# Kernel tuning notes

Hardware: AMD Instinct MI355X
Metric: run time of the kernel (lower is better)

Reference implementation:

```python
import jax, jax.numpy as jnp
import numpy as np

D_MODEL = 256
NHEAD = 8
D_K = D_MODEL // NHEAD
IM_SIZE = 8
SCALE = float(IM_SIZE ** 2)  # sqrt(im_size**4)


def setup_inputs() -> dict:
    key = jax.random.key(0)
    ks = jax.random.split(key, 9)
    B, P, S = 8, 256, 8
    s = 1.0 / np.sqrt(D_MODEL)
    return {
        "x": jax.random.normal(ks[0], (B, P, S, S, D_MODEL), jnp.float32),
        "Wq": jax.random.normal(ks[1], (D_MODEL, D_MODEL), jnp.float32) * s,
        "bq": jax.random.normal(ks[2], (D_MODEL,), jnp.float32) * s,
        "Wk": jax.random.normal(ks[3], (D_MODEL, D_MODEL), jnp.float32) * s,
        "bk": jax.random.normal(ks[4], (D_MODEL,), jnp.float32) * s,
        "Wv": jax.random.normal(ks[5], (D_MODEL, D_MODEL), jnp.float32) * s,
        "bv": jax.random.normal(ks[6], (D_MODEL,), jnp.float32) * s,
        "Wo": jax.random.normal(ks[7], (D_MODEL, D_MODEL), jnp.float32) * s,
        "bo": jax.random.normal(ks[8], (D_MODEL,), jnp.float32) * s,
    }


def _split_heads(t):
    # torch: view(..., d_k, nhead).permute(0,5,1,2,3,4) -> [b, n, p, x, y, d_k]
    b, p, sx, sy, _ = t.shape
    t = t.reshape(b, p, sx, sy, D_K, NHEAD)
    return jnp.transpose(t, (0, 5, 1, 2, 3, 4))


def reference(x, Wq, bq, Wk, bk, Wv, bv, Wo, bo):
    Q = _split_heads(x @ Wq.T + bq)
    K = _split_heads(x @ Wk.T + bk)
    V = _split_heads(x @ Wv.T + bv)
    # scores over flattened (x, y, d_k) dims
    scores = jnp.einsum('bnpxyd,bnqxyd->bnpq', Q, K) / SCALE
    attn = jax.nn.softmax(scores, axis=-1)
    out = jnp.einsum('bnpq,bnqxyd->bnpxyd', attn, V)
    # permute to [b, p, x, y, d_k, n] then merge (d_k, n) -> d_model
    out = jnp.transpose(out, (0, 2, 3, 4, 5, 1))
    b, p, sx, sy, _, _ = out.shape
    out = out.reshape(b, p, sx, sy, NHEAD * D_K)
    return out @ Wo.T + bo
```

## Files before the change

kernel.cpp:

```cpp
#include <hip/hip_runtime.h>
#include <hip/hip_bf16.h>


typedef __bf16 bf16;
typedef __attribute__((ext_vector_type(8))) __bf16 bf16x8;
typedef __attribute__((ext_vector_type(4))) float floatx4;
typedef __attribute__((ext_vector_type(8))) unsigned short ushort8;

#define CDIM 2048

static __device__ __forceinline__ floatx4 mfma16(bf16x8 a, bf16x8 b, floatx4 c) {
  return __builtin_amdgcn_mfma_f32_16x16x32_bf16(a, b, c, 0, 0, 0);
}

static __device__ __forceinline__ void gload_lds16(const void* g, void* l) {
  __builtin_amdgcn_global_load_lds((const __attribute__((address_space(1))) void*)g,
                                   (__attribute__((address_space(3))) void*)l, 16, 0, 0);
}

__global__ __launch_bounds__(256) void k0_prep(
    const float* __restrict__ Wq, const float* __restrict__ bq,
    const float* __restrict__ Wk, const float* __restrict__ bk,
    const float* __restrict__ Wv, const float* __restrict__ bv,
    const float* __restrict__ Wo,
    bf16* __restrict__ Wp, bf16* __restrict__ Wk3, float* __restrict__ biasp)
{
  const int bid = blockIdx.x, tid = threadIdx.x;
  int g = (bid & 31) * 256 + tid;
  int lane = g & 63, rowblk = (g >> 6) & 15, kk = g >> 10;
  int h = lane >> 4, cl = lane & 15;
  int d0 = kk * 32 + 8 * h;
  if (bid < 32) {
    int ip = rowblk * 16 + cl;
    int isrc = ((ip & 31) << 3) | (ip >> 5);
#pragma unroll
    for (int mat = 0; mat < 3; mat++) {
      const float* W = (mat == 0) ? Wq : (mat == 1) ? Wk : Wv;
      bf16x8 v;
#pragma unroll
      for (int j = 0; j < 8; j++) v[j] = (bf16)W[isrc * 256 + d0 + j];
      *reinterpret_cast<bf16x8*>(Wp + ((size_t)mat * 8192 + g) * 8) = v;
    }
    if (bid == 0 && tid < 256) {
      int bs = ((tid & 31) << 3) | (tid >> 5);
      biasp[tid] = bq[bs]; biasp[256 + tid] = bk[bs]; biasp[512 + tid] = bv[bs];
    }
  } else {
    int j = rowblk * 16 + cl;
    bf16x8 v;
#pragma unroll
    for (int jj = 0; jj < 8; jj++) {
      int c = d0 + jj;
      v[jj] = (bf16)Wo[j * 256 + (((c & 31) << 3) | (c >> 5))];
    }
    *reinterpret_cast<bf16x8*>(Wk3 + (size_t)g * 8) = v;
  }
}

__global__ __launch_bounds__(512, 4) void k1_qkv(
    const float* __restrict__ x, const bf16* __restrict__ Wp,
    const float* __restrict__ biasp,
    bf16* __restrict__ Qs, bf16* __restrict__ Ks, bf16* __restrict__ Vt)
{
  __shared__ bf16 buf[2][64 * 256];
  const int bx = blockIdx.x;
  const int tid = threadIdx.x;
  const int lane = tid & 63;
  const int w = tid >> 6;
  const int h = lane >> 4, cl = lane & 15;
  const int c7 = cl & 7;

  floatx4 sreg[8];

#define K1_LOAD(VB)                                                          \
  {                                                                          \
    int a_ = (VB) / 24;                                                      \
    int t0_ = (a_ * 8 + ((VB) & 7)) * 64;                                    \
    _Pragma("unroll")                                                        \
    for (int k = 0; k < 4; ++k) {                                            \
      int G = k * 512 + tid;                                                 \
      int row = G >> 5;                                                      \
      const float* sp = x + (size_t)(t0_ + row) * 256 + (G & 31) * 8;        \
      sreg[2 * k]     = *reinterpret_cast<const floatx4*>(sp);               \
      sreg[2 * k + 1] = *reinterpret_cast<const floatx4*>(sp + 4);           \
    }                                                                        \
  }

#define K1_CVTWRITE(BUFI)                                                    \
  {                                                                          \
    _Pragma("unroll")                                                        \
    for (int k = 0; k < 4; ++k) {                                            \
      int G = k * 512 + tid;                                                 \
      int row = G >> 5;                                                      \
      bf16x8 v;                                                              \
      _Pragma("unroll")                                                      \
      for (int j = 0; j < 4; j++) {                                          \
        v[j] = (bf16)sreg[2 * k][j];                                         \
        v[4 + j] = (bf16)sreg[2 * k + 1][j];                                 \
      }                                                                      \
      int Gp = (G & ~7) | ((G ^ row) & 7);                                   \
      *reinterpret_cast<bf16x8*>(&buf[BUFI][Gp * 8]) = v;                    \
    }                                                                        \
  }

#define K1_COMPUTE(VB, BUFI)                                                 \
  {                                                                          \
    int a_ = (VB) / 24;                                                      \
    int rem_ = (VB) - a_ * 24;                                               \
    int mat_ = rem_ >> 3;                                                    \
    int t0_ = (a_ * 8 + (rem_ & 7)) * 64;                                    \
    const bf16* Wm = Wp + (size_t)mat_ * 65536;                              \
    floatx4 acc[4][2];                                                       \
    _Pragma("unroll")                                                        \
    for (int i = 0; i < 4; i++)                                              \
      _Pragma("unroll")                                                      \
      for (int j = 0; j < 2; j++) acc[i][j] = (floatx4)0.0f;                 \
    _Pragma("unroll 2")                                                      \
    for (int kk = 0; kk < 8; ++kk) {                                         \
      bf16x8 av[4];                                                          \
      _Pragma("unroll")                                                      \
      for (int mt = 0; mt < 4; mt++) {                                       \
        int rr = mt * 16 + cl;                                               \
        int G = rr * 32 + kk * 4 + h;                                        \
        int Gp = (G & ~7) | ((G ^ c7) & 7);                                  \
        av[mt] = *reinterpret_cast<const bf16x8*>(&buf[BUFI][Gp * 8]);       \
      }                                                                      \
      bf16x8 b0 = *reinterpret_cast<const bf16x8*>(                          \
          Wm + ((size_t)(kk * 16 + w * 2 + 0) * 64 + lane) * 8);             \
      bf16x8 b1 = *reinterpret_cast<const bf16x8*>(                          \
          Wm + ((size_t)(kk * 16 + w * 2 + 1) * 64 + lane) * 8);             \
      _Pragma("unroll")                                                      \
      for (int mt = 0; mt < 4; mt++) acc[mt][0] = mfma16(av[mt], b0, acc[mt][0]); \
      _Pragma("unroll")                                                      \
      for (int mt = 0; mt < 4; mt++) acc[mt][1] = mfma16(av[mt], b1, acc[mt][1]); \
    }                                                                        \
    int b_ = t0_ >> 14;                                                      \
    int p_ = (t0_ >> 6) & 255;                                               \
    if (mat_ < 2) {                                                          \
      bf16* ob = ((mat_ == 0) ? Qs : Ks) + ((size_t)(b_ * 8 + w) * 256 + p_) * 2048; \
      _Pragma("unroll")                                                      \
      for (int nt = 0; nt < 2; nt++) {                                       \
        const int ip = w * 32 + nt * 16 + cl;                                \
        const float bb = biasp[mat_ * 256 + ip];                             \
        const int dk = nt * 16 + cl;                                         \
        _Pragma("unroll")                                                    \
        for (int mt = 0; mt < 4; mt++)                                       \
          _Pragma("unroll")                                                  \
          for (int r = 0; r < 4; r++) {                                      \
            int sxy = mt * 16 + 4 * h + r;                                   \
            ob[sxy * 32 + dk] = (bf16)(acc[mt][nt][r] + bb);                 \
          }                                                                  \
      }                                                                      \
    } else {                                                                 \
      _Pragma("unroll")                                                      \
      for (int nt = 0; nt < 2; nt++) {                                       \
        const int ip = w * 32 + nt * 16 + cl;                                \
        const float bb = biasp[512 + ip];                                    \
        _Pragma("unroll")                                                    \
        for (int mt = 0; mt < 4; mt++)                                       \
          _Pragma("unroll")                                                  \
          for (int r = 0; r < 4; r++) {                                      \
            int t = t0_ + mt * 16 + 4 * h + r;                               \
            Vt[(size_t)t * 256 + ip] = (bf16)(acc[mt][nt][r] + bb);          \
          }                                                                  \
      }                                                                      \
    }                                                                        \
  }

  K1_LOAD(bx);
  K1_CVTWRITE(0);
  __syncthreads();
#pragma unroll
  for (int u = 1; u < 4; ++u) {
    K1_LOAD(bx + u * 1536);
    K1_COMPUTE(bx + (u - 1) * 1536, (u - 1) & 1);
    __syncthreads();
    K1_CVTWRITE(u & 1);
    __syncthreads();
  }
  K1_COMPUTE(bx + 3 * 1536, 1);

#undef K1_LOAD
#undef K1_CVTWRITE
#undef K1_COMPUTE
}

__global__ __launch_bounds__(1024, 4) void k2a_scores(
    const bf16* __restrict__ Qs, const bf16* __restrict__ Ks,
    bf16* __restrict__ attn)
{
  __shared__ bf16 Qch[2][128 * 64];
  __shared__ bf16 Kch[2][256 * 64];
  __shared__ float redmax[4][4][32];
  __shared__ float redsum[4][4][32];

  const int bx = blockIdx.x;
  const int bn = bx & 63;
  const int p0 = (bx >> 6) * 128;
  const int tid = threadIdx.x;
  const int lane = tid & 63;
  const int w = tid >> 6;
  const int wr = w >> 2, wc = w & 3;
  const int h = lane >> 4, cl = lane & 15;

  const bf16* Qb = Qs + (size_t)bn * 524288 + (size_t)p0 * 2048;
  const bf16* Kb = Ks + (size_t)bn * 524288;

  const int Lq = w * 64 + lane;
  const int rq = Lq >> 3, sq = (Lq & 7) ^ (rq & 7);
  const size_t qsrc = (size_t)rq * 2048 + sq * 8;
  int rk[2]; size_t ksrc[2];
#pragma unroll
  for (int i = 0; i < 2; ++i) {
    int L = i * 1024 + w * 64 + lane;
    rk[i] = L >> 3;
    int s = (L & 7) ^ (rk[i] & 7);
    ksrc[i] = (size_t)rk[i] * 2048 + s * 8;
  }

#define K2A_STAGE(bufi, c)                                                  \
  {                                                                         \
    gload_lds16(Qb + qsrc + (c) * 64, &Qch[bufi][(w * 64) * 8]);            \
    gload_lds16(Kb + ksrc[0] + (c) * 64, &Kch[bufi][(w * 64) * 8]);         \
    gload_lds16(Kb + ksrc[1] + (c) * 64, &Kch[bufi][(1024 + w * 64) * 8]);  \
  }

  floatx4 acc[2][4];
#pragma unroll
  for (int i = 0; i < 2; i++)
#pragma unroll
    for (int j = 0; j < 4; j++) acc[i][j] = (floatx4)0.0f;

  K2A_STAGE(0, 0);
  __syncthreads();
  int buf = 0;
  for (int c = 0; c < 32; ++c) {
    if (c + 1 < 32) K2A_STAGE(buf ^ 1, c + 1);
#pragma unroll
    for (int kk = 0; kk < 2; ++kk) {
      bf16x8 av[2], bv[4];
#pragma unroll
      for (int mt = 0; mt < 2; mt++) {
        int row = wr * 32 + mt * 16 + cl;
        int gg = kk * 4 + h;
        av[mt] = *reinterpret_cast<const bf16x8*>(
            &Qch[buf][(row * 8 + (gg ^ (row & 7))) * 8]);
      }
#pragma unroll
      for (int nt = 0; nt < 4; nt++) {
        int row = wc * 64 + nt * 16 + cl;
        int gg = kk * 4 + h;
        bv[nt] = *reinterpret_cast<const bf16x8*>(
            &Kch[buf][(row * 8 + (gg ^ (row & 7))) * 8]);
      }
#pragma unroll
      for (int nt = 0; nt < 4; nt++)
#pragma unroll
        for (int mt = 0; mt < 2; mt++)
          acc[mt][nt] = mfma16(av[mt], bv[nt], acc[mt][nt]);
    }
    __syncthreads();
    buf ^= 1;
  }

  float pm[2][4];
#pragma unroll
  for (int mt = 0; mt < 2; mt++)
#pragma unroll
    for (int r = 0; r < 4; r++)
      pm[mt][r] = fmaxf(fmaxf(acc[mt][0][r], acc[mt][1][r]),
                        fmaxf(acc[mt][2][r], acc[mt][3][r]));
#pragma unroll
  for (int off = 1; off < 16; off <<= 1)
#pragma unroll
    for (int mt = 0; mt < 2; mt++)
#pragma unroll
      for (int r = 0; r < 4; r++)
        pm[mt][r] = fmaxf(pm[mt][r], __shfl_xor(pm[mt][r], off, 64));
  if (cl == 0) {
#pragma unroll
    for (int mt = 0; mt < 2; mt++)
#pragma unroll
      for (int r = 0; r < 4; r++) redmax[wr][wc][mt * 16 + 4 * h + r] = pm[mt][r];
  }
  __syncthreads();

  float gm[2][4], ps[2][4];
#pragma unroll
  for (int mt = 0; mt < 2; mt++)
#pragma unroll
    for (int r = 0; r < 4; r++) {
      int row = mt * 16 + 4 * h + r;
      gm[mt][r] = fmaxf(fmaxf(redmax[wr][0][row], redmax[wr][1][row]),
                        fmaxf(redmax[wr][2][row], redmax[wr][3][row]));
      ps[mt][r] = 0.0f;
    }
  const float KS = 1.44269504088896340736f / 64.0f;
#pragma unroll
  for (int mt = 0; mt < 2; mt++)
#pragma unroll
    for (int nt = 0; nt < 4; nt++)
#pragma unroll
      for (int r = 0; r < 4; r++) {
        float e = exp2f((acc[mt][nt][r] - gm[mt][r]) * KS);
        acc[mt][nt][r] = e;
        ps[mt][r] += e;
      }
#pragma unroll
  for (int off = 1; off < 16; off <<= 1)
#pragma unroll
    for (int mt = 0; mt < 2; mt++)
#pragma unroll
      for (int r = 0; r < 4; r++) ps[mt][r] += __shfl_xor(ps[mt][r], off, 64);
  if (cl == 0) {
#pragma unroll
    for (int mt = 0; mt < 2; mt++)
#pragma unroll
      for (int r = 0; r < 4; r++) redsum[wr][wc][mt * 16 + 4 * h + r] = ps[mt][r];
  }
  __syncthreads();

#pragma unroll
  for (int mt = 0; mt < 2; mt++)
#pragma unroll
    for (int r = 0; r < 4; r++) {
      int row = mt * 16 + 4 * h + r;
      float gs = (redsum[wr][0][row] + redsum[wr][1][row])
               + (redsum[wr][2][row] + redsum[wr][3][row]);
      ps[mt][r] = 1.0f / gs;
    }
#pragma unroll
  for (int nt = 0; nt < 4; nt++) {
    int q = wc * 64 + nt * 16 + cl;
#pragma unroll
    for (int mt = 0; mt < 2; mt++)
#pragma unroll
      for (int r = 0; r < 4; r++) {
        int row = p0 + wr * 32 + mt * 16 + 4 * h + r;
        attn[(size_t)bn * 65536 + row * 256 + q] = (bf16)(acc[mt][nt][r] * ps[mt][r]);
      }
  }
#undef K2A_STAGE
}

__global__ __launch_bounds__(256) void k2t_transpose(
    const bf16* __restrict__ Vtok, bf16* __restrict__ Vq)
{
  const int bx = blockIdx.x;
  const int bn = bx & 63;
  const int r2 = bx >> 6;
  const int q0 = (r2 & 3) * 64;
  const int c0 = (r2 >> 2) * 64;
  const int b = bn >> 3, n = bn & 7;
  __shared__ unsigned short tile[64][65];
  const unsigned short* src = (const unsigned short*)Vtok;
  unsigned short* dst = (unsigned short*)Vq + (size_t)bn * 524288;
  {
    const int q = threadIdx.x >> 3;
    const int cj = (threadIdx.x & 7) * 8;
    const int c = c0 + cj;
    const int sxy = c >> 5, dk0 = c & 31;
#pragma unroll
    for (int it = 0; it < 2; ++it) {
      int qq = q + it * 32;
      size_t sa = (size_t)((b * 256 + q0 + qq) * 64 + sxy) * 256 + n * 32 + dk0;
      ushort8 s = *reinterpret_cast<const ushort8*>(src + sa);
#pragma unroll
      for (int j = 0; j < 8; j++) tile[qq][cj + j] = s[j];
    }
  }
  __syncthreads();
  {
    const int crow = threadIdx.x >> 2;
    const int qj = (threadIdx.x & 3) * 8;
#pragma unroll
    for (int it = 0; it < 2; ++it) {
      int qq = qj + it * 32;
      ushort8 sv;
#pragma unroll
      for (int j = 0; j < 8; j++) sv[j] = tile[qq + j][crow];
      *reinterpret_cast<ushort8*>(dst + (size_t)(c0 + crow) * 256 + q0 + qq) = sv;
    }
  }
}

__global__ __launch_bounds__(512, 6) void k2b_pv(
    const bf16* __restrict__ attn, const bf16* __restrict__ Vq,
    bf16* __restrict__ yhat)
{
  __shared__ bf16 As[64 * 256];
  const int bx = blockIdx.x;
  const int bn = bx & 63;
  const int r2 = bx >> 6;
  const int p0 = (r2 & 3) * 64;
  const int c0 = (r2 >> 2) * 256;
  const int b = bn >> 3, n = bn & 7;
  const int tid = threadIdx.x;
  const int lane = tid & 63;
  const int w = tid >> 6;
  const int h = lane >> 4, cl = lane & 15;
  const int c7 = cl & 7;

  const bf16* Ab = attn + (size_t)bn * 65536 + (size_t)p0 * 256;
  const bf16* Vb = Vq + (size_t)bn * 524288;

#pragma unroll
  for (int i = 0; i < 4; ++i) {
    int L = (i * 8 + w) * 64 + lane;
    int S = (L & ~7) | ((L ^ (L >> 5)) & 7);
    gload_lds16(Ab + (size_t)S * 8, &As[(size_t)(i * 8 + w) * 64 * 8]);
  }
  __syncthreads();

  floatx4 acc[4][2];
#pragma unroll
  for (int i = 0; i < 4; i++)
#pragma unroll
    for (int j = 0; j < 2; j++) acc[i][j] = (floatx4)0.0f;

#pragma unroll 2
  for (int kk = 0; kk < 8; ++kk) {
    bf16x8 av[4];
#pragma unroll
    for (int mt = 0; mt < 4; mt++) {
      int rr = mt * 16 + cl;
      int G = rr * 32 + kk * 4 + h;
      int Gp = (G & ~7) | ((G ^ c7) & 7);
      av[mt] = *reinterpret_cast<const bf16x8*>(&As[Gp * 8]);
    }
    bf16x8 b0 = *reinterpret_cast<const bf16x8*>(
        Vb + (size_t)(c0 + w * 32 + cl) * 256 + kk * 32 + 8 * h);
    bf16x8 b1 = *reinterpret_cast<const bf16x8*>(
        Vb + (size_t)(c0 + w * 32 + 16 + cl) * 256 + kk * 32 + 8 * h);
#pragma unroll
    for (int mt = 0; mt < 4; mt++) acc[mt][0] = mfma16(av[mt], b0, acc[mt][0]);
#pragma unroll
    for (int mt = 0; mt < 4; mt++) acc[mt][1] = mfma16(av[mt], b1, acc[mt][1]);
  }

#pragma unroll
  for (int nt = 0; nt < 2; nt++) {
    const int cg = c0 + w * 32 + nt * 16 + cl;
    const int dk = cg & 31, sxy = cg >> 5;
#pragma unroll
    for (int mt = 0; mt < 4; mt++)
#pragma unroll
      for (int r = 0; r < 4; r++) {
        int p = p0 + mt * 16 + 4 * h + r;
        size_t t = (size_t)((b * 256 + p) * 64) + sxy;
        yhat[t * 256 + n * 32 + dk] = (bf16)acc[mt][nt][r];
      }
  }
}

__global__ __launch_bounds__(512, 6) void k3_out(
    const bf16* __restrict__ yhat, const bf16* __restrict__ Wk3,
    const float* __restrict__ bo, float* __restrict__ outp)
{
  __shared__ bf16 As[64 * 256];
  const int t0 = blockIdx.x * 64;
  const int tid = threadIdx.x;
  const int lane = tid & 63;
  const int w = tid >> 6;
  const int h = lane >> 4, cl = lane & 15;
  const int c7 = cl & 7;

  const bf16* Ab = yhat + (size_t)t0 * 256;

#pragma unroll
  for (int i = 0; i < 4; ++i) {
    int L = (i * 8 + w) * 64 + lane;
    int S = (L & ~7) | ((L ^ (L >> 5)) & 7);
    gload_lds16(Ab + (size_t)S * 8, &As[(size_t)(i * 8 + w) * 64 * 8]);
  }
  __syncthreads();

  floatx4 acc[4][2];
#pragma unroll
  for (int i = 0; i < 4; i++)
#pragma unroll
    for (int j = 0; j < 2; j++) acc[i][j] = (floatx4)0.0f;

#pragma unroll 2
  for (int kk = 0; kk < 8; ++kk) {
    bf16x8 av[4];
#pragma unroll
    for (int mt = 0; mt < 4; mt++) {
      int rr = mt * 16 + cl;
      int G = rr * 32 + kk * 4 + h;
      int Gp = (G & ~7) | ((G ^ c7) & 7);
      av[mt] = *reinterpret_cast<const bf16x8*>(&As[Gp * 8]);
    }
    bf16x8 b0 = *reinterpret_cast<const bf16x8*>(
        Wk3 + ((size_t)(kk * 16 + w * 2 + 0) * 64 + lane) * 8);
    bf16x8 b1 = *reinterpret_cast<const bf16x8*>(
        Wk3 + ((size_t)(kk * 16 + w * 2 + 1) * 64 + lane) * 8);
#pragma unroll
    for (int mt = 0; mt < 4; mt++) acc[mt][0] = mfma16(av[mt], b0, acc[mt][0]);
#pragma unroll
    for (int mt = 0; mt < 4; mt++) acc[mt][1] = mfma16(av[mt], b1, acc[mt][1]);
  }

#pragma unroll
  for (int nt = 0; nt < 2; nt++) {
    const int j = w * 32 + nt * 16 + cl;
    const float bb = bo[j];
#pragma unroll
    for (int mt = 0; mt < 4; mt++)
#pragma unroll
      for (int r = 0; r < 4; r++)
        outp[(size_t)(t0 + mt * 16 + 4 * h + r) * 256 + j] = acc[mt][nt][r] + bb;
  }
}

extern "C" void kernel_launch(void* const* d_in, const int* in_sizes, int n_in,
                              void* d_out, int out_size, void* d_ws, size_t ws_size,
                              hipStream_t stream) {
  const float* x  = (const float*)d_in[0];
  const float* Wq = (const float*)d_in[1];
  const float* bq = (const float*)d_in[2];
  const float* Wk = (const float*)d_in[3];
  const float* bk = (const float*)d_in[4];
  const float* Wv = (const float*)d_in[5];
  const float* bv = (const float*)d_in[6];
  const float* Wo = (const float*)d_in[7];
  const float* bo = (const float*)d_in[8];
  float* outp = (float*)d_out;

  char* ws = (char*)d_ws;
  const size_t SZ_QKV = 67108864;
  size_t off = 0;
  bf16* Qs   = (bf16*)(ws + off); off += SZ_QKV;
  bf16* Ks   = (bf16*)(ws + off); off += SZ_QKV;
  bf16* Vtok = (bf16*)(ws + off); off += SZ_QKV;
  bf16* attn = (bf16*)(ws + off); off += 8388608;
  bf16* Wp   = (bf16*)(ws + off); off += 393216;
  bf16* Wk3  = (bf16*)(ws + off); off += 131072;
  float* biasp = (float*)(ws + off); off += 3072;
  if (ws_size < off) return;

  bf16* yhat = Qs;
  bf16* Vq   = Ks;

  k0_prep<<<64, 256, 0, stream>>>(Wq, bq, Wk, bk, Wv, bv, Wo, Wp, Wk3, biasp);
  k1_qkv<<<1536, 512, 0, stream>>>(x, Wp, biasp, Qs, Ks, Vtok);
  k2a_scores<<<128, 1024, 0, stream>>>(Qs, Ks, attn);
  k2t_transpose<<<8192, 256, 0, stream>>>(Vtok, Vq);
  k2b_pv<<<2048, 512, 0, stream>>>(attn, Vq, yhat);
  k3_out<<<2048, 512, 0, stream>>>(yhat, Wk3, bo, outp);
}
```

Measured before the change: 311.9 us.

## Fuse scores, softmax and PV into one attention kernel per head

Replaces the separate scores/softmax kernel and PV kernel with one kernel. Each 1024-thread block handles 64 query rows: it computes QK^T, applies softmax, keeps the probabilities in shared memory and multiplies them by V. This removes the global attn round trip and one launch. In exchange the grid is only 256 blocks, and each block streams all of V for its head, so V is re-read once per query tile. The workspace now needs a separate Vq buffer, and the QKV projection unroll goes from 2 to 4.

```diff
diff --git a/kernel.cpp b/kernel.cpp
--- a/kernel.cpp
+++ b/kernel.cpp
@@ -115,7 +115,7 @@
     for (int i = 0; i < 4; i++)                                              \
       _Pragma("unroll")                                                      \
       for (int j = 0; j < 2; j++) acc[i][j] = (floatx4)0.0f;                 \
-    _Pragma("unroll 2")                                                      \
+    _Pragma("unroll 4")                                                      \
     for (int kk = 0; kk < 8; ++kk) {                                         \
       bf16x8 av[4];                                                          \
       _Pragma("unroll")                                                      \
@@ -183,164 +183,6 @@
 #undef K1_LOAD
 #undef K1_CVTWRITE
 #undef K1_COMPUTE
-}
-
-__global__ __launch_bounds__(1024, 4) void k2a_scores(
-    const bf16* __restrict__ Qs, const bf16* __restrict__ Ks,
-    bf16* __restrict__ attn)
-{
-  __shared__ bf16 Qch[2][128 * 64];
-  __shared__ bf16 Kch[2][256 * 64];
-  __shared__ float redmax[4][4][32];
-  __shared__ float redsum[4][4][32];
-
-  const int bx = blockIdx.x;
-  const int bn = bx & 63;
-  const int p0 = (bx >> 6) * 128;
-  const int tid = threadIdx.x;
-  const int lane = tid & 63;
-  const int w = tid >> 6;
-  const int wr = w >> 2, wc = w & 3;
-  const int h = lane >> 4, cl = lane & 15;
-
-  const bf16* Qb = Qs + (size_t)bn * 524288 + (size_t)p0 * 2048;
-  const bf16* Kb = Ks + (size_t)bn * 524288;
-
-  const int Lq = w * 64 + lane;
-  const int rq = Lq >> 3, sq = (Lq & 7) ^ (rq & 7);
-  const size_t qsrc = (size_t)rq * 2048 + sq * 8;
-  int rk[2]; size_t ksrc[2];
-#pragma unroll
-  for (int i = 0; i < 2; ++i) {
-    int L = i * 1024 + w * 64 + lane;
-    rk[i] = L >> 3;
-    int s = (L & 7) ^ (rk[i] & 7);
-    ksrc[i] = (size_t)rk[i] * 2048 + s * 8;
-  }
-
-#define K2A_STAGE(bufi, c)                                                  \
-  {                                                                         \
-    gload_lds16(Qb + qsrc + (c) * 64, &Qch[bufi][(w * 64) * 8]);            \
-    gload_lds16(Kb + ksrc[0] + (c) * 64, &Kch[bufi][(w * 64) * 8]);         \
-    gload_lds16(Kb + ksrc[1] + (c) * 64, &Kch[bufi][(1024 + w * 64) * 8]);  \
-  }
-
-  floatx4 acc[2][4];
-#pragma unroll
-  for (int i = 0; i < 2; i++)
-#pragma unroll
-    for (int j = 0; j < 4; j++) acc[i][j] = (floatx4)0.0f;
-
-  K2A_STAGE(0, 0);
-  __syncthreads();
-  int buf = 0;
-  for (int c = 0; c < 32; ++c) {
-    if (c + 1 < 32) K2A_STAGE(buf ^ 1, c + 1);
-#pragma unroll
-    for (int kk = 0; kk < 2; ++kk) {
-      bf16x8 av[2], bv[4];
-#pragma unroll
-      for (int mt = 0; mt < 2; mt++) {
-        int row = wr * 32 + mt * 16 + cl;
-        int gg = kk * 4 + h;
-        av[mt] = *reinterpret_cast<const bf16x8*>(
-            &Qch[buf][(row * 8 + (gg ^ (row & 7))) * 8]);
-      }
-#pragma unroll
-      for (int nt = 0; nt < 4; nt++) {
-        int row = wc * 64 + nt * 16 + cl;
-        int gg = kk * 4 + h;
-        bv[nt] = *reinterpret_cast<const bf16x8*>(
-            &Kch[buf][(row * 8 + (gg ^ (row & 7))) * 8]);
-      }
-#pragma unroll
-      for (int nt = 0; nt < 4; nt++)
-#pragma unroll
-        for (int mt = 0; mt < 2; mt++)
-          acc[mt][nt] = mfma16(av[mt], bv[nt], acc[mt][nt]);
-    }
-    __syncthreads();
-    buf ^= 1;
-  }
-
-  float pm[2][4];
-#pragma unroll
-  for (int mt = 0; mt < 2; mt++)
-#pragma unroll
-    for (int r = 0; r < 4; r++)
-      pm[mt][r] = fmaxf(fmaxf(acc[mt][0][r], acc[mt][1][r]),
-                        fmaxf(acc[mt][2][r], acc[mt][3][r]));
-#pragma unroll
-  for (int off = 1; off < 16; off <<= 1)
-#pragma unroll
-    for (int mt = 0; mt < 2; mt++)
-#pragma unroll
-      for (int r = 0; r < 4; r++)
-        pm[mt][r] = fmaxf(pm[mt][r], __shfl_xor(pm[mt][r], off, 64));
-  if (cl == 0) {
-#pragma unroll
-    for (int mt = 0; mt < 2; mt++)
-#pragma unroll
-      for (int r = 0; r < 4; r++) redmax[wr][wc][mt * 16 + 4 * h + r] = pm[mt][r];
-  }
-  __syncthreads();
-
-  float gm[2][4], ps[2][4];
-#pragma unroll
-  for (int mt = 0; mt < 2; mt++)
-#pragma unroll
-    for (int r = 0; r < 4; r++) {
-      int row = mt * 16 + 4 * h + r;
-      gm[mt][r] = fmaxf(fmaxf(redmax[wr][0][row], redmax[wr][1][row]),
-                        fmaxf(redmax[wr][2][row], redmax[wr][3][row]));
-      ps[mt][r] = 0.0f;
-    }
-  const float KS = 1.44269504088896340736f / 64.0f;
-#pragma unroll
-  for (int mt = 0; mt < 2; mt++)
-#pragma unroll
-    for (int nt = 0; nt < 4; nt++)
-#pragma unroll
-      for (int r = 0; r < 4; r++) {
-        float e = exp2f((acc[mt][nt][r] - gm[mt][r]) * KS);
-        acc[mt][nt][r] = e;
-        ps[mt][r] += e;
-      }
-#pragma unroll
-  for (int off = 1; off < 16; off <<= 1)
-#pragma unroll
-    for (int mt = 0; mt < 2; mt++)
-#pragma unroll
-      for (int r = 0; r < 4; r++) ps[mt][r] += __shfl_xor(ps[mt][r], off, 64);
-  if (cl == 0) {
-#pragma unroll
-    for (int mt = 0; mt < 2; mt++)
-#pragma unroll
-      for (int r = 0; r < 4; r++) redsum[wr][wc][mt * 16 + 4 * h + r] = ps[mt][r];
-  }
-  __syncthreads();
-
-#pragma unroll
-  for (int mt = 0; mt < 2; mt++)
-#pragma unroll
-    for (int r = 0; r < 4; r++) {
-      int row = mt * 16 + 4 * h + r;
-      float gs = (redsum[wr][0][row] + redsum[wr][1][row])
-               + (redsum[wr][2][row] + redsum[wr][3][row]);
-      ps[mt][r] = 1.0f / gs;
-    }
-#pragma unroll
-  for (int nt = 0; nt < 4; nt++) {
-    int q = wc * 64 + nt * 16 + cl;
-#pragma unroll
-    for (int mt = 0; mt < 2; mt++)
-#pragma unroll
-      for (int r = 0; r < 4; r++) {
-        int row = p0 + wr * 32 + mt * 16 + 4 * h + r;
-        attn[(size_t)bn * 65536 + row * 256 + q] = (bf16)(acc[mt][nt][r] * ps[mt][r]);
-      }
-  }
-#undef K2A_STAGE
 }
 
 __global__ __launch_bounds__(256) void k2t_transpose(
@@ -384,73 +226,181 @@
   }
 }
 
-__global__ __launch_bounds__(512, 6) void k2b_pv(
-    const bf16* __restrict__ attn, const bf16* __restrict__ Vq,
-    bf16* __restrict__ yhat)
+__global__ __launch_bounds__(1024, 4) void k2f_attn(
+    const bf16* __restrict__ Qs, const bf16* __restrict__ Ks,
+    const bf16* __restrict__ Vq, bf16* __restrict__ yhat)
 {
-  __shared__ bf16 As[64 * 256];
+  __shared__ __align__(16) bf16 smem[49152];
+  __shared__ float redmax[4][4][16];
+  __shared__ float redsum[4][4][16];
+
   const int bx = blockIdx.x;
   const int bn = bx & 63;
-  const int r2 = bx >> 6;
-  const int p0 = (r2 & 3) * 64;
-  const int c0 = (r2 >> 2) * 256;
-  const int b = bn >> 3, n = bn & 7;
+  const int p0 = (bx >> 6) * 64;
   const int tid = threadIdx.x;
   const int lane = tid & 63;
   const int w = tid >> 6;
+  const int wr = w >> 2, wc = w & 3;
   const int h = lane >> 4, cl = lane & 15;
-  const int c7 = cl & 7;
-
-  const bf16* Ab = attn + (size_t)bn * 65536 + (size_t)p0 * 256;
+  const int b = bn >> 3, n = bn & 7;
+
+  const bf16* Qb = Qs + (size_t)bn * 524288 + (size_t)p0 * 2048;
+  const bf16* Kb = Ks + (size_t)bn * 524288;
   const bf16* Vb = Vq + (size_t)bn * 524288;
 
-#pragma unroll
-  for (int i = 0; i < 4; ++i) {
-    int L = (i * 8 + w) * 64 + lane;
-    int S = (L & ~7) | ((L ^ (L >> 5)) & 7);
-    gload_lds16(Ab + (size_t)S * 8, &As[(size_t)(i * 8 + w) * 64 * 8]);
-  }
-  __syncthreads();
-
-  floatx4 acc[4][2];
-#pragma unroll
-  for (int i = 0; i < 4; i++)
-#pragma unroll
-    for (int j = 0; j < 2; j++) acc[i][j] = (floatx4)0.0f;
-
+  const int Lq = tid;
+  const int rq = Lq >> 3, sq = (Lq & 7) ^ (rq & 7);
+  const size_t qsrc = (size_t)rq * 2048 + sq * 8;
+  int rk[2]; size_t ksrc[2];
+#pragma unroll
+  for (int i = 0; i < 2; ++i) {
+    int L = i * 1024 + tid;
+    rk[i] = L >> 3;
+    int s = (L & 7) ^ (rk[i] & 7);
+    ksrc[i] = (size_t)rk[i] * 2048 + s * 8;
+  }
+
+#define QCH(bufi) (smem + (bufi) * 4096)
+#define KCH(bufi) (smem + 8192 + (bufi) * 16384)
+
+#define K2F_STAGE(bufi, c)                                                   \
+  {                                                                          \
+    if (tid < 512) gload_lds16(Qb + qsrc + (c) * 64, QCH(bufi) + (w * 64) * 8); \
+    gload_lds16(Kb + ksrc[0] + (c) * 64, KCH(bufi) + (w * 64) * 8);          \
+    gload_lds16(Kb + ksrc[1] + (c) * 64, KCH(bufi) + (1024 + w * 64) * 8);   \
+  }
+
+  floatx4 acc[4];
+#pragma unroll
+  for (int j = 0; j < 4; j++) acc[j] = (floatx4)0.0f;
+
+  K2F_STAGE(0, 0);
+  __syncthreads();
+  int buf = 0;
+  for (int c = 0; c < 32; ++c) {
+    if (c + 1 < 32) K2F_STAGE(buf ^ 1, c + 1);
+#pragma unroll
+    for (int kk = 0; kk < 2; ++kk) {
+      bf16x8 av, bv[4];
+      {
+        int row = wr * 16 + cl;
+        int gg = kk * 4 + h;
+        av = *reinterpret_cast<const bf16x8*>(
+            QCH(buf) + (row * 8 + (gg ^ (row & 7))) * 8);
+      }
+#pragma unroll
+      for (int nt = 0; nt < 4; nt++) {
+        int row = wc * 64 + nt * 16 + cl;
+        int gg = kk * 4 + h;
+        bv[nt] = *reinterpret_cast<const bf16x8*>(
+            KCH(buf) + (row * 8 + (gg ^ (row & 7))) * 8);
+      }
+#pragma unroll
+      for (int nt = 0; nt < 4; nt++) acc[nt] = mfma16(av, bv[nt], acc[nt]);
+    }
+    __syncthreads();
+    buf ^= 1;
+  }
+
+  float pm[4];
+#pragma unroll
+  for (int r = 0; r < 4; r++)
+    pm[r] = fmaxf(fmaxf(acc[0][r], acc[1][r]), fmaxf(acc[2][r], acc[3][r]));
+#pragma unroll
+  for (int off = 1; off < 16; off <<= 1)
+#pragma unroll
+    for (int r = 0; r < 4; r++)
+      pm[r] = fmaxf(pm[r], __shfl_xor(pm[r], off, 64));
+  if (cl == 0) {
+#pragma unroll
+    for (int r = 0; r < 4; r++) redmax[wr][wc][4 * h + r] = pm[r];
+  }
+  __syncthreads();
+
+  float gm[4], ps[4];
+#pragma unroll
+  for (int r = 0; r < 4; r++) {
+    int row = 4 * h + r;
+    gm[r] = fmaxf(fmaxf(redmax[wr][0][row], redmax[wr][1][row]),
+                  fmaxf(redmax[wr][2][row], redmax[wr][3][row]));
+    ps[r] = 0.0f;
+  }
+  const float KS = 1.44269504088896340736f / 64.0f;
+#pragma unroll
+  for (int nt = 0; nt < 4; nt++)
+#pragma unroll
+    for (int r = 0; r < 4; r++) {
+      float e = exp2f((acc[nt][r] - gm[r]) * KS);
+      acc[nt][r] = e;
+      ps[r] += e;
+    }
+#pragma unroll
+  for (int off = 1; off < 16; off <<= 1)
+#pragma unroll
+    for (int r = 0; r < 4; r++) ps[r] += __shfl_xor(ps[r], off, 64);
+  if (cl == 0) {
+#pragma unroll
+    for (int r = 0; r < 4; r++) redsum[wr][wc][4 * h + r] = ps[r];
+  }
+  __syncthreads();
+
+#pragma unroll
+  for (int r = 0; r < 4; r++) {
+    int row = 4 * h + r;
+    float gs = (redsum[wr][0][row] + redsum[wr][1][row])
+             + (redsum[wr][2][row] + redsum[wr][3][row]);
+    ps[r] = 1.0f / gs;
+  }
+
+#pragma unroll
+  for (int nt = 0; nt < 4; nt++) {
+    int q = wc * 64 + nt * 16 + cl;
+    int g = q >> 3, qi = q & 7;
+#pragma unroll
+    for (int r = 0; r < 4; r++) {
+      int row = wr * 16 + 4 * h + r;
+      int gp = (g & ~7) | ((g ^ (row & 7)) & 7);
+      smem[row * 256 + gp * 8 + qi] = (bf16)(acc[nt][r] * ps[r]);
+    }
+  }
+  __syncthreads();
+
+  for (int cc = 0; cc < 8; ++cc) {
+    floatx4 a2[4];
+#pragma unroll
+    for (int j = 0; j < 4; j++) a2[j] = (floatx4)0.0f;
 #pragma unroll 2
-  for (int kk = 0; kk < 8; ++kk) {
-    bf16x8 av[4];
-#pragma unroll
-    for (int mt = 0; mt < 4; mt++) {
-      int rr = mt * 16 + cl;
-      int G = rr * 32 + kk * 4 + h;
-      int Gp = (G & ~7) | ((G ^ c7) & 7);
-      av[mt] = *reinterpret_cast<const bf16x8*>(&As[Gp * 8]);
-    }
-    bf16x8 b0 = *reinterpret_cast<const bf16x8*>(
-        Vb + (size_t)(c0 + w * 32 + cl) * 256 + kk * 32 + 8 * h);
-    bf16x8 b1 = *reinterpret_cast<const bf16x8*>(
-        Vb + (size_t)(c0 + w * 32 + 16 + cl) * 256 + kk * 32 + 8 * h);
-#pragma unroll
-    for (int mt = 0; mt < 4; mt++) acc[mt][0] = mfma16(av[mt], b0, acc[mt][0]);
-#pragma unroll
-    for (int mt = 0; mt < 4; mt++) acc[mt][1] = mfma16(av[mt], b1, acc[mt][1]);
-  }
-
-#pragma unroll
-  for (int nt = 0; nt < 2; nt++) {
-    const int cg = c0 + w * 32 + nt * 16 + cl;
-    const int dk = cg & 31, sxy = cg >> 5;
-#pragma unroll
-    for (int mt = 0; mt < 4; mt++)
+    for (int kk = 0; kk < 8; ++kk) {
+      bf16x8 av;
+      {
+        int row = wr * 16 + cl;
+        int gg = kk * 4 + h;
+        av = *reinterpret_cast<const bf16x8*>(
+            smem + (row * 32 + ((gg & ~7) | ((gg ^ (row & 7)) & 7))) * 8);
+      }
+#pragma unroll
+      for (int nt = 0; nt < 4; nt++) {
+        int cr = cc * 256 + wc * 64 + nt * 16 + cl;
+        bf16x8 bv = *reinterpret_cast<const bf16x8*>(
+            Vb + (size_t)cr * 256 + kk * 32 + 8 * h);
+        a2[nt] = mfma16(av, bv, a2[nt]);
+      }
+    }
+#pragma unroll
+    for (int nt = 0; nt < 4; nt++) {
+      const int cg = cc * 256 + wc * 64 + nt * 16 + cl;
+      const int dk = cg & 31, sxy = cg >> 5;
 #pragma unroll
       for (int r = 0; r < 4; r++) {
-        int p = p0 + mt * 16 + 4 * h + r;
+        int p = p0 + wr * 16 + 4 * h + r;
         size_t t = (size_t)((b * 256 + p) * 64) + sxy;
-        yhat[t * 256 + n * 32 + dk] = (bf16)acc[mt][nt][r];
+        yhat[t * 256 + n * 32 + dk] = (bf16)a2[nt][r];
       }
-  }
+    }
+  }
+#undef QCH
+#undef KCH
+#undef K2F_STAGE
 }
 
 __global__ __launch_bounds__(512, 6) void k3_out(
@@ -533,19 +483,17 @@
   bf16* Qs   = (bf16*)(ws + off); off += SZ_QKV;
   bf16* Ks   = (bf16*)(ws + off); off += SZ_QKV;
   bf16* Vtok = (bf16*)(ws + off); off += SZ_QKV;
-  bf16* attn = (bf16*)(ws + off); off += 8388608;
+  bf16* Vq   = (bf16*)(ws + off); off += SZ_QKV;
   bf16* Wp   = (bf16*)(ws + off); off += 393216;
   bf16* Wk3  = (bf16*)(ws + off); off += 131072;
   float* biasp = (float*)(ws + off); off += 3072;
   if (ws_size < off) return;
 
-  bf16* yhat = Qs;
-  bf16* Vq   = Ks;
+  bf16* yhat = Vtok;
 
   k0_prep<<<64, 256, 0, stream>>>(Wq, bq, Wk, bk, Wv, bv, Wo, Wp, Wk3, biasp);
   k1_qkv<<<1536, 512, 0, stream>>>(x, Wp, biasp, Qs, Ks, Vtok);
-  k2a_scores<<<128, 1024, 0, stream>>>(Qs, Ks, attn);
   k2t_transpose<<<8192, 256, 0, stream>>>(Vtok, Vq);
-  k2b_pv<<<2048, 512, 0, stream>>>(attn, Vq, yhat);
+  k2f_attn<<<256, 1024, 0, stream>>>(Qs, Ks, Vq, yhat);
   k3_out<<<2048, 512, 0, stream>>>(yhat, Wk3, bo, outp);
 }
```

Result: slower. 416.0 us (+33.4%).

## Halve scores row tile for more blocks; keep V in registers across p-tiles in PV

Applied to the files above, without the earlier changes.

The scores kernel now gives each block 64 query rows instead of 128, doubling the grid from 128 to 256 blocks so more of the GPU's compute units have work. The cost is that each K chunk is loaded twice as often. The PV kernel now loops over all four p-tiles inside one block and holds its V fragments in registers, so V is read from global memory once instead of four times. This cuts the PV grid to 512 blocks and adds per-thread register pressure.

```diff
diff --git a/kernel.cpp b/kernel.cpp
--- a/kernel.cpp
+++ b/kernel.cpp
@@ -185,18 +185,18 @@
 #undef K1_COMPUTE
 }
 
-__global__ __launch_bounds__(1024, 4) void k2a_scores(
+__global__ __launch_bounds__(1024, 1) void k2a_scores(
     const bf16* __restrict__ Qs, const bf16* __restrict__ Ks,
     bf16* __restrict__ attn)
 {
-  __shared__ bf16 Qch[2][128 * 64];
+  __shared__ bf16 Qch[2][64 * 64];
   __shared__ bf16 Kch[2][256 * 64];
-  __shared__ float redmax[4][4][32];
-  __shared__ float redsum[4][4][32];
+  __shared__ float redmax[4][4][16];
+  __shared__ float redsum[4][4][16];
 
   const int bx = blockIdx.x;
   const int bn = bx & 63;
-  const int p0 = (bx >> 6) * 128;
+  const int p0 = (bx >> 6) * 64;
   const int tid = threadIdx.x;
   const int lane = tid & 63;
   const int w = tid >> 6;
@@ -206,13 +206,12 @@
   const bf16* Qb = Qs + (size_t)bn * 524288 + (size_t)p0 * 2048;
   const bf16* Kb = Ks + (size_t)bn * 524288;
 
-  const int Lq = w * 64 + lane;
-  const int rq = Lq >> 3, sq = (Lq & 7) ^ (rq & 7);
+  const int rq = tid >> 3, sq = (tid & 7) ^ (rq & 7);
   const size_t qsrc = (size_t)rq * 2048 + sq * 8;
   int rk[2]; size_t ksrc[2];
 #pragma unroll
   for (int i = 0; i < 2; ++i) {
-    int L = i * 1024 + w * 64 + lane;
+    int L = i * 1024 + tid;
     rk[i] = L >> 3;
     int s = (L & 7) ^ (rk[i] & 7);
     ksrc[i] = (size_t)rk[i] * 2048 + s * 8;
@@ -220,16 +219,14 @@
 
 #define K2A_STAGE(bufi, c)                                                  \
   {                                                                         \
-    gload_lds16(Qb + qsrc + (c) * 64, &Qch[bufi][(w * 64) * 8]);            \
+    if (tid < 512) gload_lds16(Qb + qsrc + (c) * 64, &Qch[bufi][(w * 64) * 8]); \
     gload_lds16(Kb + ksrc[0] + (c) * 64, &Kch[bufi][(w * 64) * 8]);         \
     gload_lds16(Kb + ksrc[1] + (c) * 64, &Kch[bufi][(1024 + w * 64) * 8]);  \
   }
 
-  floatx4 acc[2][4];
-#pragma unroll
-  for (int i = 0; i < 2; i++)
-#pragma unroll
-    for (int j = 0; j < 4; j++) acc[i][j] = (floatx4)0.0f;
+  floatx4 acc[4];
+#pragma unroll
+  for (int j = 0; j < 4; j++) acc[j] = (floatx4)0.0f;
 
   K2A_STAGE(0, 0);
   __syncthreads();
@@ -238,12 +235,11 @@
     if (c + 1 < 32) K2A_STAGE(buf ^ 1, c + 1);
 #pragma unroll
     for (int kk = 0; kk < 2; ++kk) {
-      bf16x8 av[2], bv[4];
-#pragma unroll
-      for (int mt = 0; mt < 2; mt++) {
-        int row = wr * 32 + mt * 16 + cl;
+      bf16x8 av, bv[4];
+      {
+        int row = wr * 16 + cl;
         int gg = kk * 4 + h;
-        av[mt] = *reinterpret_cast<const bf16x8*>(
+        av = *reinterpret_cast<const bf16x8*>(
             &Qch[buf][(row * 8 + (gg ^ (row & 7))) * 8]);
       }
 #pragma unroll
@@ -254,91 +250,69 @@
             &Kch[buf][(row * 8 + (gg ^ (row & 7))) * 8]);
       }
 #pragma unroll
-      for (int nt = 0; nt < 4; nt++)
-#pragma unroll
-        for (int mt = 0; mt < 2; mt++)
-          acc[mt][nt] = mfma16(av[mt], bv[nt], acc[mt][nt]);
+      for (int nt = 0; nt < 4; nt++) acc[nt] = mfma16(av, bv[nt], acc[nt]);
     }
     __syncthreads();
     buf ^= 1;
   }
 
-  float pm[2][4];
-#pragma unroll
-  for (int mt = 0; mt < 2; mt++)
+  float pm[4];
+#pragma unroll
+  for (int r = 0; r < 4; r++)
+    pm[r] = fmaxf(fmaxf(acc[0][r], acc[1][r]), fmaxf(acc[2][r], acc[3][r]));
+#pragma unroll
+  for (int off = 1; off < 16; off <<= 1)
 #pragma unroll
     for (int r = 0; r < 4; r++)
-      pm[mt][r] = fmaxf(fmaxf(acc[mt][0][r], acc[mt][1][r]),
-                        fmaxf(acc[mt][2][r], acc[mt][3][r]));
+      pm[r] = fmaxf(pm[r], __shfl_xor(pm[r], off, 64));
+  if (cl == 0) {
+#pragma unroll
+    for (int r = 0; r < 4; r++) redmax[wr][wc][4 * h + r] = pm[r];
+  }
+  __syncthreads();
+
+  float gm[4], ps[4];
+#pragma unroll
+  for (int r = 0; r < 4; r++) {
+    int row = 4 * h + r;
+    gm[r] = fmaxf(fmaxf(redmax[wr][0][row], redmax[wr][1][row]),
+                  fmaxf(redmax[wr][2][row], redmax[wr][3][row]));
+    ps[r] = 0.0f;
+  }
+  const float KS = 1.44269504088896340736f / 64.0f;
+#pragma unroll
+  for (int nt = 0; nt < 4; nt++)
+#pragma unroll
+    for (int r = 0; r < 4; r++) {
+      float e = exp2f((acc[nt][r] - gm[r]) * KS);
+      acc[nt][r] = e;
+      ps[r] += e;
+    }
 #pragma unroll
   for (int off = 1; off < 16; off <<= 1)
 #pragma unroll
-    for (int mt = 0; mt < 2; mt++)
-#pragma unroll
-      for (int r = 0; r < 4; r++)
-        pm[mt][r] = fmaxf(pm[mt][r], __shfl_xor(pm[mt][r], off, 64));
+    for (int r = 0; r < 4; r++) ps[r] += __shfl_xor(ps[r], off, 64);
   if (cl == 0) {
 #pragma unroll
-    for (int mt = 0; mt < 2; mt++)
-#pragma unroll
-      for (int r = 0; r < 4; r++) redmax[wr][wc][mt * 16 + 4 * h + r] = pm[mt][r];
+    for (int r = 0; r < 4; r++) redsum[wr][wc][4 * h + r] = ps[r];
   }
   __syncthreads();
 
-  float gm[2][4], ps[2][4];
-#pragma unroll
-  for (int mt = 0; mt < 2; mt++)
-#pragma unroll
-    for (int r = 0; r < 4; r++) {
-      int row = mt * 16 + 4 * h + r;
-      gm[mt][r] = fmaxf(fmaxf(redmax[wr][0][row], redmax[wr][1][row]),
-                        fmaxf(redmax[wr][2][row], redmax[wr][3][row]));
-      ps[mt][r] = 0.0f;
-    }
-  const float KS = 1.44269504088896340736f / 64.0f;
-#pragma unroll
-  for (int mt = 0; mt < 2; mt++)
-#pragma unroll
-    for (int nt = 0; nt < 4; nt++)
-#pragma unroll
-      for (int r = 0; r < 4; r++) {
-        float e = exp2f((acc[mt][nt][r] - gm[mt][r]) * KS);
-        acc[mt][nt][r] = e;
-        ps[mt][r] += e;
-      }
-#pragma unroll
-  for (int off = 1; off < 16; off <<= 1)
-#pragma unroll
-    for (int mt = 0; mt < 2; mt++)
-#pragma unroll
-      for (int r = 0; r < 4; r++) ps[mt][r] += __shfl_xor(ps[mt][r], off, 64);
-  if (cl == 0) {
-#pragma unroll
-    for (int mt = 0; mt < 2; mt++)
-#pragma unroll
-      for (int r = 0; r < 4; r++) redsum[wr][wc][mt * 16 + 4 * h + r] = ps[mt][r];
-  }
-  __syncthreads();
-
-#pragma unroll
-  for (int mt = 0; mt < 2; mt++)
-#pragma unroll
-    for (int r = 0; r < 4; r++) {
-      int row = mt * 16 + 4 * h + r;
-      float gs = (redsum[wr][0][row] + redsum[wr][1][row])
-               + (redsum[wr][2][row] + redsum[wr][3][row]);
-      ps[mt][r] = 1.0f / gs;
-    }
+#pragma unroll
+  for (int r = 0; r < 4; r++) {
+    int row = 4 * h + r;
+    float gs = (redsum[wr][0][row] + redsum[wr][1][row])
+             + (redsum[wr][2][row] + redsum[wr][3][row]);
+    ps[r] = 1.0f / gs;
+  }
 #pragma unroll
   for (int nt = 0; nt < 4; nt++) {
     int q = wc * 64 + nt * 16 + cl;
 #pragma unroll
-    for (int mt = 0; mt < 2; mt++)
-#pragma unroll
-      for (int r = 0; r < 4; r++) {
-        int row = p0 + wr * 32 + mt * 16 + 4 * h + r;
-        attn[(size_t)bn * 65536 + row * 256 + q] = (bf16)(acc[mt][nt][r] * ps[mt][r]);
-      }
+    for (int r = 0; r < 4; r++) {
+      int row = p0 + wr * 16 + 4 * h + r;
+      attn[(size_t)bn * 65536 + row * 256 + q] = (bf16)(acc[nt][r] * ps[r]);
+    }
   }
 #undef K2A_STAGE
 }
@@ -384,16 +358,14 @@
   }
 }
 
-__global__ __launch_bounds__(512, 6) void k2b_pv(
+__global__ __launch_bounds__(512, 4) void k2b_pv(
     const bf16* __restrict__ attn, const bf16* __restrict__ Vq,
     bf16* __restrict__ yhat)
 {
   __shared__ bf16 As[64 * 256];
   const int bx = blockIdx.x;
   const int bn = bx & 63;
-  const int r2 = bx >> 6;
-  const int p0 = (r2 & 3) * 64;
-  const int c0 = (r2 >> 2) * 256;
+  const int c0 = (bx >> 6) * 256;
   const int b = bn >> 3, n = bn & 7;
   const int tid = threadIdx.x;
   const int lane = tid & 63;
@@ -401,55 +373,64 @@
   const int h = lane >> 4, cl = lane & 15;
   const int c7 = cl & 7;
 
-  const bf16* Ab = attn + (size_t)bn * 65536 + (size_t)p0 * 256;
   const bf16* Vb = Vq + (size_t)bn * 524288;
 
-#pragma unroll
-  for (int i = 0; i < 4; ++i) {
-    int L = (i * 8 + w) * 64 + lane;
-    int S = (L & ~7) | ((L ^ (L >> 5)) & 7);
-    gload_lds16(Ab + (size_t)S * 8, &As[(size_t)(i * 8 + w) * 64 * 8]);
-  }
-  __syncthreads();
-
-  floatx4 acc[4][2];
-#pragma unroll
-  for (int i = 0; i < 4; i++)
-#pragma unroll
-    for (int j = 0; j < 2; j++) acc[i][j] = (floatx4)0.0f;
+  bf16x8 breg[8][2];
+#pragma unroll
+  for (int kk = 0; kk < 8; ++kk)
+#pragma unroll
+    for (int j = 0; j < 2; ++j)
+      breg[kk][j] = *reinterpret_cast<const bf16x8*>(
+          Vb + (size_t)(c0 + w * 32 + j * 16 + cl) * 256 + kk * 32 + 8 * h);
+
+  for (int pt = 0; pt < 4; ++pt) {
+    const int p0 = pt * 64;
+    const bf16* Ab = attn + (size_t)bn * 65536 + (size_t)p0 * 256;
+
+#pragma unroll
+    for (int i = 0; i < 4; ++i) {
+      int L = (i * 8 + w) * 64 + lane;
+      int S = (L & ~7) | ((L ^ (L >> 5)) & 7);
+      gload_lds16(Ab + (size_t)S * 8, &As[(size_t)(i * 8 + w) * 64 * 8]);
+    }
+    __syncthreads();
+
+    floatx4 acc[4][2];
+#pragma unroll
+    for (int i = 0; i < 4; i++)
+#pragma unroll
+      for (int j = 0; j < 2; j++) acc[i][j] = (floatx4)0.0f;
 
 #pragma unroll 2
-  for (int kk = 0; kk < 8; ++kk) {
-    bf16x8 av[4];
-#pragma unroll
-    for (int mt = 0; mt < 4; mt++) {
-      int rr = mt * 16 + cl;
-      int G = rr * 32 + kk * 4 + h;
-      int Gp = (G & ~7) | ((G ^ c7) & 7);
-      av[mt] = *reinterpret_cast<const bf16x8*>(&As[Gp * 8]);
-    }
-    bf16x8 b0 = *reinterpret_cast<const bf16x8*>(
-        Vb + (size_t)(c0 + w * 32 + cl) * 256 + kk * 32 + 8 * h);
-    bf16x8 b1 = *reinterpret_cast<const bf16x8*>(
-        Vb + (size_t)(c0 + w * 32 + 16 + cl) * 256 + kk * 32 + 8 * h);
-#pragma unroll
-    for (int mt = 0; mt < 4; mt++) acc[mt][0] = mfma16(av[mt], b0, acc[mt][0]);
-#pragma unroll
-    for (int mt = 0; mt < 4; mt++) acc[mt][1] = mfma16(av[mt], b1, acc[mt][1]);
-  }
-
-#pragma unroll
-  for (int nt = 0; nt < 2; nt++) {
-    const int cg = c0 + w * 32 + nt * 16 + cl;
-    const int dk = cg & 31, sxy = cg >> 5;
-#pragma unroll
-    for (int mt = 0; mt < 4; mt++)
-#pragma unroll
-      for (int r = 0; r < 4; r++) {
-        int p = p0 + mt * 16 + 4 * h + r;
-        size_t t = (size_t)((b * 256 + p) * 64) + sxy;
-        yhat[t * 256 + n * 32 + dk] = (bf16)acc[mt][nt][r];
+    for (int kk = 0; kk < 8; ++kk) {
+      bf16x8 av[4];
+#pragma unroll
+      for (int mt = 0; mt < 4; mt++) {
+        int rr = mt * 16 + cl;
+        int G = rr * 32 + kk * 4 + h;
+        int Gp = (G & ~7) | ((G ^ c7) & 7);
+        av[mt] = *reinterpret_cast<const bf16x8*>(&As[Gp * 8]);
       }
+#pragma unroll
+      for (int mt = 0; mt < 4; mt++) acc[mt][0] = mfma16(av[mt], breg[kk][0], acc[mt][0]);
+#pragma unroll
+      for (int mt = 0; mt < 4; mt++) acc[mt][1] = mfma16(av[mt], breg[kk][1], acc[mt][1]);
+    }
+
+#pragma unroll
+    for (int nt = 0; nt < 2; nt++) {
+      const int cg = c0 + w * 32 + nt * 16 + cl;
+      const int dk = cg & 31, sxy = cg >> 5;
+#pragma unroll
+      for (int mt = 0; mt < 4; mt++)
+#pragma unroll
+        for (int r = 0; r < 4; r++) {
+          int p = p0 + mt * 16 + 4 * h + r;
+          size_t t = (size_t)((b * 256 + p) * 64) + sxy;
+          yhat[t * 256 + n * 32 + dk] = (bf16)acc[mt][nt][r];
+        }
+    }
+    __syncthreads();
   }
 }
 
@@ -544,8 +525,8 @@
 
   k0_prep<<<64, 256, 0, stream>>>(Wq, bq, Wk, bk, Wv, bv, Wo, Wp, Wk3, biasp);
   k1_qkv<<<1536, 512, 0, stream>>>(x, Wp, biasp, Qs, Ks, Vtok);
-  k2a_scores<<<128, 1024, 0, stream>>>(Qs, Ks, attn);
+  k2a_scores<<<256, 1024, 0, stream>>>(Qs, Ks, attn);
   k2t_transpose<<<8192, 256, 0, stream>>>(Vtok, Vq);
-  k2b_pv<<<2048, 512, 0, stream>>>(attn, Vq, yhat);
+  k2b_pv<<<512, 512, 0, stream>>>(attn, Vq, yhat);
   k3_out<<<2048, 512, 0, stream>>>(yhat, Wk3, bo, outp);
 }
```

After: 338.5 us. 8.5% more time.
